# Optimization experiments

Measured on AMD Instinct MI355X. Metric: run time of the kernel, lower is better.

Reference implementation:

```python
import jax, jax.numpy as jnp
import numpy as np

N = 100000
E = 1600000
L = 128   # latent_size
H = 128   # hidden_size
O = 128   # output_size


def setup_inputs() -> dict:
    key = jax.random.key(0)
    ks = jax.random.split(key, 16)
    s = 1.0 / np.sqrt(H)
    inp = {
        "z": jax.random.normal(ks[0], (N, L), dtype=jnp.float32),
        "edge_index": jax.random.randint(ks[1], (2, E), 0, N, dtype=jnp.int64),
        # LSTM params (torch order: i, f, g, o)
        "W_ih": jax.random.uniform(ks[2], (4 * H, L), jnp.float32, -s, s),
        "W_hh": jax.random.uniform(ks[3], (4 * H, H), jnp.float32, -s, s),
        "b_ih": jax.random.uniform(ks[4], (4 * H,), jnp.float32, -s, s),
        "b_hh": jax.random.uniform(ks[5], (4 * H,), jnp.float32, -s, s),
        # GCNConv weights (x @ W + b)
        "W1": jax.random.uniform(ks[6], (H, H), jnp.float32, -s, s),
        "b1": jnp.zeros((H,), jnp.float32),
        "W2": jax.random.uniform(ks[7], (H, H), jnp.float32, -s, s),
        "b2": jnp.zeros((H,), jnp.float32),
        # final Linear
        "W3": jax.random.uniform(ks[8], (O, H), jnp.float32, -s, s),
        "b3": jax.random.uniform(ks[9], (O,), jnp.float32, -s, s),
    }
    return inp


def _gcn_conv(x, W, b, src, dst, norm, n_nodes):
    # x: [N, H]; src/dst/norm: [E+N] (self-loops included)
    h = x @ W                                   # [N, H] transform first (H==H)
    msg = h[src] * norm[:, None]                # gather + edge scale
    out = jax.ops.segment_sum(msg, dst, num_segments=n_nodes)  # scatter-add
    return out + b


def _lstm_step(z, W_ih, W_hh, b_ih, b_hh):
    # single time-step, h0 = c0 = 0
    gates = z @ W_ih.T + (jnp.zeros((1, H), z.dtype) @ W_hh.T) + b_ih + b_hh
    i, f, g, o = jnp.split(gates, 4, axis=-1)
    c = jax.nn.sigmoid(i) * jnp.tanh(g)         # f * c0 == 0
    return jax.nn.sigmoid(o) * jnp.tanh(c)


def reference(z, edge_index, W_ih, W_hh, b_ih, b_hh, W1, b1, W2, b2, W3, b3):
    n = z.shape[0]
    # add self-loops (PyG GCNConv default)
    loop = jnp.arange(n, dtype=edge_index.dtype)
    src = jnp.concatenate([edge_index[0], loop])
    dst = jnp.concatenate([edge_index[1], loop])
    # symmetric normalization: deg from dst (incoming, incl. self-loop)
    deg = jax.ops.segment_sum(jnp.ones_like(dst, dtype=z.dtype), dst, num_segments=n)
    dinv = jnp.where(deg > 0, jax.lax.rsqrt(deg), 0.0)
    norm = dinv[src] * dinv[dst]

    h = _lstm_step(z, W_ih, W_hh, b_ih, b_hh)
    x = jax.nn.relu(_gcn_conv(h, W1, b1, src, dst, norm, n))
    x = _gcn_conv(x, W2, b2, src, dst, norm, n)
    return jax.nn.relu(x @ W3.T + b3)
```

## Files before the change

kernel.cpp:

```cpp
#include <hip/hip_runtime.h>
#include <math.h>

typedef __attribute__((ext_vector_type(8))) short short8;
typedef __attribute__((ext_vector_type(4))) float floatx4;

#define HDIM 128
#define NPB 256
#define BKMAX 1024
#define CHUNK 8192
#define STAGE_CAP 8192

__device__ __forceinline__ float bf2f(unsigned short u) {
    unsigned int x = ((unsigned int)u) << 16;
    float f;
    __builtin_memcpy(&f, &x, 4);
    return f;
}
__device__ __forceinline__ unsigned short f2bf(float f) {
    unsigned int x;
    __builtin_memcpy(&x, &f, 4);
    unsigned int r = (x + 0x7fffu + ((x >> 16) & 1u)) >> 16;
    return (unsigned short)r;
}
__device__ __forceinline__ void split1(float v, unsigned short& hi, unsigned short& lo) {
    unsigned int x;
    __builtin_memcpy(&x, &v, 4);
    hi = (unsigned short)(x >> 16);
    lo = f2bf(v - bf2f(hi));
}
__device__ __forceinline__ float fast_sigmoid(float x) {
    return 1.0f / (1.0f + __expf(-x));
}
__device__ __forceinline__ float fast_tanh(float x) {
    float ax = fabsf(x);
    float e = __expf(2.0f * ax);
    float t = 1.0f - 2.0f / (e + 1.0f);
    return copysignf(t, x);
}

__device__ __forceinline__ void gload_lds16(const void* g, void* lds) {
    __builtin_amdgcn_global_load_lds(
        (const __attribute__((address_space(1))) unsigned int*)g,
        (__attribute__((address_space(3))) unsigned int*)lds, 16, 0, 0);
}

__global__ void prep_weights_kernel(const float* __restrict__ Wih,
                                    const float* __restrict__ W1,
                                    const float* __restrict__ bih,
                                    const float* __restrict__ bhh,
                                    unsigned short* __restrict__ Wihh, unsigned short* __restrict__ Wihl,
                                    unsigned short* __restrict__ W1h,  unsigned short* __restrict__ W1l,
                                    float* __restrict__ bsum) {
    int i = blockIdx.x * 256 + threadIdx.x;
    unsigned short h, l;
    if (i < 65536) {
        split1(Wih[i], h, l);
        Wihh[i] = h; Wihl[i] = l;
    } else if (i < 81920) {
        int t = i - 65536, r = t >> 7, c = t & 127;
        split1(W1[r * HDIM + c], h, l);
        W1h[c * HDIM + r] = h; W1l[c * HDIM + r] = l;
    } else if (i < 82432) {
        int t = i - 81920;
        bsum[t] = bih[t] + bhh[t];
    }
}

__global__ void prep_w23_kernel(const float* __restrict__ W2,
                                const float* __restrict__ W3,
                                const float* __restrict__ b2,
                                const float* __restrict__ b3,
                                unsigned short* __restrict__ W23h,
                                unsigned short* __restrict__ W23l,
                                float* __restrict__ b23) {
    int i = blockIdx.x * 256 + threadIdx.x;
    if (i < 16384) {
        int n = i >> 7, k = i & 127;
        float s = 0.0f;
#pragma unroll 8
        for (int p = 0; p < 128; ++p)
            s += W2[k * HDIM + p] * W3[n * HDIM + p];
        unsigned short h, l;
        split1(s, h, l);
        W23h[n * HDIM + k] = h;
        W23l[n * HDIM + k] = l;
    } else if (i < 16512) {
        int n = i - 16384;
        float s = b3[n];
#pragma unroll 8
        for (int p = 0; p < 128; ++p)
            s += b2[p] * W3[n * HDIM + p];
        b23[n] = s;
    }
}

__global__ __launch_bounds__(256)
void bucket_hist_kernel(const int* __restrict__ ei, int* __restrict__ bcnt,
                        long E, int K) {
    __shared__ int h[BKMAX];
    const int tid = threadIdx.x;
    for (int i = tid; i < K; i += 256) h[i] = 0;
    __syncthreads();
    const long base = (long)blockIdx.x * CHUNK;
#pragma unroll
    for (int j = 0; j < CHUNK / 256; ++j) {
        long e = base + j * 256 + tid;
        if (e < E) atomicAdd(&h[((unsigned)ei[E + e]) >> 8], 1);
    }
    __syncthreads();
    for (int i = tid; i < K; i += 256) {
        int c = h[i];
        if (c) atomicAdd(&bcnt[i], c);
    }
}

__global__ __launch_bounds__(1024)
void scan_buckets_kernel(const int* __restrict__ bcnt, int* __restrict__ gbase,
                         int* __restrict__ gcur, int* __restrict__ offs,
                         int K, int N, int Etot) {
    __shared__ int buf[1024];
    const int t = threadIdx.x;
    const int v = (t < K) ? bcnt[t] : 0;
    buf[t] = v;
    __syncthreads();
    for (int off = 1; off < 1024; off <<= 1) {
        int x = buf[t];
        int y = (t >= off) ? buf[t - off] : 0;
        __syncthreads();
        buf[t] = x + y;
        __syncthreads();
    }
    if (t < K) { gbase[t] = buf[t] - v; gcur[t] = buf[t] - v; }
    if (t == 0) { gbase[K] = Etot; offs[N] = Etot; }
}

__global__ __launch_bounds__(256)
void pair_scatter_kernel(const int* __restrict__ ei, int* __restrict__ gcur,
                         unsigned int* __restrict__ pairs, long E, int K) {
    __shared__ int h[BKMAX];
    __shared__ int cur[BKMAX];
    const int tid = threadIdx.x;
    for (int i = tid; i < K; i += 256) h[i] = 0;
    __syncthreads();
    const long base = (long)blockIdx.x * CHUNK;
#pragma unroll
    for (int j = 0; j < CHUNK / 256; ++j) {
        long e = base + j * 256 + tid;
        if (e < E) atomicAdd(&h[((unsigned)ei[E + e]) >> 8], 1);
    }
    __syncthreads();
    for (int i = tid; i < K; i += 256) {
        int c = h[i];
        cur[i] = c ? atomicAdd(&gcur[i], c) : 0;
    }
    __syncthreads();
#pragma unroll
    for (int j = 0; j < CHUNK / 256; ++j) {
        long e = base + j * 256 + tid;
        if (e < E) {
            unsigned int s = (unsigned int)ei[e];
            unsigned int d = (unsigned int)ei[E + e];
            int b = d >> 8;
            int pos = atomicAdd(&cur[b], 1);
            pairs[pos] = s | ((d & (NPB - 1)) << 24);
        }
    }
}

__global__ __launch_bounds__(256)
void bucket_csr_kernel(const unsigned int* __restrict__ pairs, const int* __restrict__ gbase,
                       int* __restrict__ offs, float* __restrict__ dinv,
                       int* __restrict__ srclist, int N) {
    __shared__ int cnt[NPB];
    __shared__ int red[NPB];
    __shared__ int cur[NPB];
    __shared__ int stage[STAGE_CAP];
    const int tid = threadIdx.x;
    const int b = blockIdx.x;
    const int node0 = b << 8;
    const int nn = min(NPB, N - node0);
    const int ebeg = gbase[b];
    const int eend = gbase[b + 1];
    const int ne = eend - ebeg;

    cnt[tid] = 0;
    __syncthreads();
    for (int i = tid; i < ne; i += 256)
        atomicAdd(&cnt[pairs[ebeg + i] >> 24], 1);
    __syncthreads();
    const int myc = cnt[tid];
    red[tid] = myc;
    __syncthreads();
    for (int off = 1; off < NPB; off <<= 1) {
        int x = red[tid];
        int y = (tid >= off) ? red[tid - off] : 0;
        __syncthreads();
        red[tid] = x + y;
        __syncthreads();
    }
    const int loff = red[tid] - myc;
    if (tid < nn) {
        offs[node0 + tid] = ebeg + loff;
        dinv[node0 + tid] = rsqrtf((float)myc + 1.0f);
    }
    cur[tid] = loff;
    __syncthreads();

    if (ne <= STAGE_CAP) {
        for (int i = tid; i < ne; i += 256) {
            unsigned int p = pairs[ebeg + i];
            int pos = atomicAdd(&cur[p >> 24], 1);
            stage[pos] = (int)(p & 0xFFFFFFu);
        }
        __syncthreads();
        for (int i = tid; i < ne; i += 256)
            srclist[ebeg + i] = stage[i];
    } else {
        for (int i = tid; i < ne; i += 256) {
            unsigned int p = pairs[ebeg + i];
            int pos = atomicAdd(&cur[p >> 24], 1);
            srclist[ebeg + pos] = (int)(p & 0xFFFFFFu);
        }
    }
}

__device__ __forceinline__ void stage_swz(const unsigned short* __restrict__ g,
                                          long rowBase, long maxRow, int kOff,
                                          unsigned short* lds, int nrows, int tid) {
    const int nchunks = nrows << 3;
    for (int L = tid; L < nchunks; L += 256) {
        int r = L >> 3, cS = L & 7;
        int cG = cS ^ (r & 7);
        long gr = rowBase + r;
        if (gr >= maxRow) gr = maxRow - 1;
        gload_lds16(g + gr * HDIM + kOff + cG * 8, lds + (long)L * 8);
    }
}
__device__ __forceinline__ int swz_off(int r, int c0) {
    return (r * 8 + (c0 ^ (r & 7))) * 8;
}

__global__ __launch_bounds__(256, 4)
void gemm_split(const unsigned short* __restrict__ Ah, const unsigned short* __restrict__ Al,
                const unsigned short* __restrict__ Bh, const unsigned short* __restrict__ Bl,
                float* __restrict__ outf, unsigned short* __restrict__ outb, long M,
                const float* __restrict__ rowScale,
                const float* __restrict__ bias, int mode)
{
    __shared__ unsigned short sBh[128 * 64], sBl[128 * 64];
    const int tid = threadIdx.x;
    const long rowBase = (long)blockIdx.x * 64;

    const int wave = tid >> 6;
    const int lane = tid & 63;
    const int quad = lane >> 4;
    const int l16  = lane & 15;
    const int arow = wave * 16 + l16;
    long ag = rowBase + arow;
    if (ag >= M) ag = M - 1;

    short8 rah[2][2], ral[2][2];
#pragma unroll
    for (int h = 0; h < 2; ++h)
#pragma unroll
        for (int kk = 0; kk < 2; ++kk) {
            const long o = ag * HDIM + h * 64 + kk * 32 + quad * 8;
            rah[h][kk] = *(const short8*)(Ah + o);
            ral[h][kk] = *(const short8*)(Al + o);
        }

    floatx4 acc[8];
#pragma unroll
    for (int i = 0; i < 8; ++i) acc[i] = (floatx4)0.0f;

    for (int h = 0; h < 2; ++h) {
        __syncthreads();
        stage_swz(Bh, 0, 128, h * 64, sBh, 128, tid);
        stage_swz(Bl, 0, 128, h * 64, sBl, 128, tid);
        __syncthreads();
#pragma unroll
        for (int kk = 0; kk < 2; ++kk) {
            const int c0 = kk * 4 + quad;
            short8 ah = rah[h][kk];
            short8 al = ral[h][kk];
#pragma unroll
            for (int ct = 0; ct < 8; ++ct) {
                const int bo = swz_off(ct * 16 + l16, c0);
                short8 bh = *(const short8*)(sBh + bo);
                short8 bl = *(const short8*)(sBl + bo);
                acc[ct] = __builtin_amdgcn_mfma_f32_16x16x32_bf16(ah, bh, acc[ct], 0, 0, 0);
                acc[ct] = __builtin_amdgcn_mfma_f32_16x16x32_bf16(ah, bl, acc[ct], 0, 0, 0);
                acc[ct] = __builtin_amdgcn_mfma_f32_16x16x32_bf16(al, bh, acc[ct], 0, 0, 0);
            }
        }
    }

#pragma unroll
    for (int ct = 0; ct < 8; ++ct) {
#pragma unroll
        for (int r = 0; r < 4; ++r) {
            long m = rowBase + wave * 16 + quad * 4 + r;
            if (m < M) {
                int n = ct * 16 + l16;
                float v = acc[ct][r];
                if (mode == 0) {
                    v *= rowScale[m];
                    outb[m * HDIM + n] = f2bf(v);
                } else {
                    v += bias[n];
                    v = fmaxf(v, 0.0f);
                    outf[m * HDIM + n] = v;
                }
            }
        }
    }
}

__global__ __launch_bounds__(256, 2)
void lstm_gemm_split(const float* __restrict__ Z,
                     const unsigned short* __restrict__ Wh, const unsigned short* __restrict__ Wl,
                     const float* __restrict__ bsum,
                     unsigned short* __restrict__ Hh, unsigned short* __restrict__ Hl, long M)
{
    __shared__ unsigned short sBh[2][128 * 64], sBl[2][128 * 64];
    const int tid = threadIdx.x;
    const long rowBase = (long)blockIdx.x * 64;

    const int wave = tid >> 6;
    const int lane = tid & 63;
    const int quad = lane >> 4;
    const int l16  = lane & 15;
    const int arow = wave * 16 + l16;
    long ag = rowBase + arow;
    if (ag >= M) ag = M - 1;

    short8 rah[2][2], ral[2][2];
#pragma unroll
    for (int h = 0; h < 2; ++h)
#pragma unroll
        for (int kk = 0; kk < 2; ++kk) {
            const float* p = Z + ag * HDIM + h * 64 + kk * 32 + quad * 8;
            float4 f0 = *(const float4*)p;
            float4 f1 = *(const float4*)(p + 4);
            float f[8] = {f0.x, f0.y, f0.z, f0.w, f1.x, f1.y, f1.z, f1.w};
#pragma unroll
            for (int e = 0; e < 8; ++e) {
                unsigned short hi, lo;
                split1(f[e], hi, lo);
                rah[h][kk][e] = (short)hi;
                ral[h][kk][e] = (short)lo;
            }
        }

    auto stage_phase = [&](int ph, int b) {
        const int g = ph >> 1, h = ph & 1;
        const int gateRow = (g == 0) ? 0 : ((g == 1) ? 256 : 384);
        const unsigned short* gh = Wh + (long)gateRow * HDIM + h * 64;
        const unsigned short* gl = Wl + (long)gateRow * HDIM + h * 64;
#pragma unroll
        for (int it = 0; it < 4; ++it) {
            int L = it * 256 + tid;
            int r = L >> 3, cS = L & 7, cG = cS ^ (r & 7);
            gload_lds16(gh + (long)r * HDIM + cG * 8, &sBh[b][L * 8]);
        }
#pragma unroll
        for (int it = 0; it < 4; ++it) {
            int L = it * 256 + tid;
            int r = L >> 3, cS = L & 7, cG = cS ^ (r & 7);
            gload_lds16(gl + (long)r * HDIM + cG * 8, &sBl[b][L * 8]);
        }
    };

    floatx4 acc[8];
    floatx4 st[8];
#pragma unroll
    for (int i = 0; i < 8; ++i) acc[i] = (floatx4)0.0f;

    stage_phase(0, 0);

#pragma unroll
    for (int ph = 0; ph < 6; ++ph) {
        const int b = ph & 1;
        if (ph < 5) stage_phase(ph + 1, b ^ 1);
        if (ph == 2) {
#pragma unroll
            for (int ct = 0; ct < 8; ++ct) {
                const float bb = bsum[ct * 16 + l16];
#pragma unroll
                for (int r = 0; r < 4; ++r)
                    st[ct][r] = fast_sigmoid(acc[ct][r] + bb);
                acc[ct] = (floatx4)0.0f;
            }
        } else if (ph == 4) {
#pragma unroll
            for (int ct = 0; ct < 8; ++ct) {
                const float bb = bsum[256 + ct * 16 + l16];
#pragma unroll
                for (int r = 0; r < 4; ++r) {
                    float cv = st[ct][r] * fast_tanh(acc[ct][r] + bb);
                    st[ct][r] = fast_tanh(cv);
                }
                acc[ct] = (floatx4)0.0f;
            }
        }
        if (ph < 5) asm volatile("s_waitcnt vmcnt(8)" ::: "memory");
        else        asm volatile("s_waitcnt vmcnt(0)" ::: "memory");
        __builtin_amdgcn_s_barrier();
        asm volatile("" ::: "memory");
        const int hh_ = ph & 1;
#pragma unroll
        for (int kk = 0; kk < 2; ++kk) {
            const int c0 = kk * 4 + quad;
            short8 a_h = rah[hh_][kk];
            short8 a_l = ral[hh_][kk];
#pragma unroll
            for (int ct = 0; ct < 8; ++ct) {
                const int bo = swz_off(ct * 16 + l16, c0);
                short8 bh = *(const short8*)(&sBh[b][0] + bo);
                short8 bl = *(const short8*)(&sBl[b][0] + bo);
                acc[ct] = __builtin_amdgcn_mfma_f32_16x16x32_bf16(a_h, bh, acc[ct], 0, 0, 0);
                acc[ct] = __builtin_amdgcn_mfma_f32_16x16x32_bf16(a_h, bl, acc[ct], 0, 0, 0);
                acc[ct] = __builtin_amdgcn_mfma_f32_16x16x32_bf16(a_l, bh, acc[ct], 0, 0, 0);
            }
        }
        asm volatile("s_waitcnt lgkmcnt(0)" ::: "memory");
        __builtin_amdgcn_s_barrier();
        asm volatile("" ::: "memory");
    }

#pragma unroll
    for (int ct = 0; ct < 8; ++ct) {
        const float bb = bsum[384 + ct * 16 + l16];
#pragma unroll
        for (int r = 0; r < 4; ++r) {
            long m = rowBase + wave * 16 + quad * 4 + r;
            if (m < M) {
                float hv = fast_sigmoid(acc[ct][r] + bb) * st[ct][r];
                unsigned short hh, hl;
                split1(hv, hh, hl);
                int n = ct * 16 + l16;
                Hh[m * HDIM + n] = hh;
                Hl[m * HDIM + n] = hl;
            }
        }
    }
}

__global__ __launch_bounds__(256, 4)
void aggregate_kernel(const unsigned short* __restrict__ t, const int* __restrict__ srclist,
                      const int* __restrict__ offs, const float* __restrict__ dinv,
                      const float* __restrict__ bias, int doRelu,
                      unsigned short* __restrict__ Xh, unsigned short* __restrict__ Xl,
                      float* __restrict__ outF, long N)
{
    long node = (long)blockIdx.x * 4 + (threadIdx.x >> 6);
    if (node >= N) return;
    const int lane = threadIdx.x & 63;
    const int c = lane * 2;
    const int beg = offs[node];
    const int end = offs[node + 1];
    float s0[8], s1[8];
#pragma unroll
    for (int q = 0; q < 8; ++q) { s0[q] = 0.0f; s1[q] = 0.0f; }
    int j = beg;
    for (; j + 8 <= end; j += 8) {
        int srcs[8];
#pragma unroll
        for (int q = 0; q < 8; ++q) srcs[q] = srclist[j + q];
        unsigned int p[8];
#pragma unroll
        for (int q = 0; q < 8; ++q) p[q] = *(const unsigned int*)(t + (long)srcs[q] * HDIM + c);
#pragma unroll
        for (int q = 0; q < 8; ++q) {
            s0[q] += bf2f((unsigned short)(p[q] & 0xffffu));
            s1[q] += bf2f((unsigned short)(p[q] >> 16));
        }
    }
    for (; j + 4 <= end; j += 4) {
        int srcs[4];
#pragma unroll
        for (int q = 0; q < 4; ++q) srcs[q] = srclist[j + q];
#pragma unroll
        for (int q = 0; q < 4; ++q) {
            unsigned int p = *(const unsigned int*)(t + (long)srcs[q] * HDIM + c);
            s0[q] += bf2f((unsigned short)(p & 0xffffu));
            s1[q] += bf2f((unsigned short)(p >> 16));
        }
    }
    for (; j < end; ++j) {
        unsigned int p = *(const unsigned int*)(t + (long)srclist[j] * HDIM + c);
        s0[0] += bf2f((unsigned short)(p & 0xffffu));
        s1[0] += bf2f((unsigned short)(p >> 16));
    }
    const unsigned int ps = *(const unsigned int*)(t + node * HDIM + c);
    s0[0] += bf2f((unsigned short)(ps & 0xffffu));
    s1[0] += bf2f((unsigned short)(ps >> 16));
    float a0 = ((s0[0] + s0[1]) + (s0[2] + s0[3])) + ((s0[4] + s0[5]) + (s0[6] + s0[7]));
    float a1 = ((s1[0] + s1[1]) + (s1[2] + s1[3])) + ((s1[4] + s1[5]) + (s1[6] + s1[7]));
    const float d = dinv[node];
    float v0 = d * a0 + bias[c];
    float v1 = d * a1 + bias[c + 1];
    if (outF) {
        v0 = fmaxf(v0, 0.0f);
        v1 = fmaxf(v1, 0.0f);
        float2 o2 = {v0, v1};
        *(float2*)(outF + node * HDIM + c) = o2;
        return;
    }
    if (doRelu) { v0 = fmaxf(v0, 0.0f); v1 = fmaxf(v1, 0.0f); }
    unsigned short h0, l0, h1, l1;
    split1(v0, h0, l0);
    split1(v1, h1, l1);
    *(unsigned int*)(Xh + node * HDIM + c) = (unsigned int)h0 | ((unsigned int)h1 << 16);
    *(unsigned int*)(Xl + node * HDIM + c) = (unsigned int)l0 | ((unsigned int)l1 << 16);
}

extern "C" void kernel_launch(void* const* d_in, const int* in_sizes, int n_in,
                              void* d_out, int out_size, void* d_ws, size_t ws_size,
                              hipStream_t stream)
{
    const float* z   = (const float*)d_in[0];
    const int*   ei  = (const int*)d_in[1];
    const float* Wih = (const float*)d_in[2];
    const float* bih = (const float*)d_in[4];
    const float* bhh = (const float*)d_in[5];
    const float* W1  = (const float*)d_in[6];
    const float* b1  = (const float*)d_in[7];
    const float* W2  = (const float*)d_in[8];
    const float* b2  = (const float*)d_in[9];
    const float* W3  = (const float*)d_in[10];
    const float* b3  = (const float*)d_in[11];
    float* out = (float*)d_out;

    const long N = in_sizes[0] / HDIM;
    const long E = in_sizes[1] / 2;
    const int  K = (int)((N + NPB - 1) / NPB);

    char* ws = (char*)d_ws;
    size_t off = 0;
    auto alloc = [&](size_t bytes) {
        char* p = ws + off;
        off += (bytes + 255) & ~(size_t)255;
        return (void*)p;
    };
    int*   bcnt    = (int*)alloc(K * 4);
    int*   gbase   = (int*)alloc((K + 1) * 4);
    int*   gcur    = (int*)alloc(K * 4);
    int*   offs    = (int*)alloc((N + 1) * 4);
    float* dinv    = (float*)alloc(N * 4);
    unsigned int* pairs = (unsigned int*)alloc(E * 4);
    int*   srclist = (int*)alloc(E * 4);
    unsigned short* P1h = (unsigned short*)alloc(N * HDIM * 2);
    unsigned short* P1l = (unsigned short*)alloc(N * HDIM * 2);
    unsigned short* P2h = (unsigned short*)alloc(N * HDIM * 2);
    unsigned short* P2l = (unsigned short*)alloc(N * HDIM * 2);
    unsigned short* Tb  = (unsigned short*)alloc(N * HDIM * 2);
    unsigned short* Wihh = (unsigned short*)alloc(512 * HDIM * 2);
    unsigned short* Wihl = (unsigned short*)alloc(512 * HDIM * 2);
    unsigned short* W1h  = (unsigned short*)alloc(HDIM * HDIM * 2);
    unsigned short* W1l  = (unsigned short*)alloc(HDIM * HDIM * 2);
    unsigned short* W23h = (unsigned short*)alloc(HDIM * HDIM * 2);
    unsigned short* W23l = (unsigned short*)alloc(HDIM * HDIM * 2);
    float* bsum = (float*)alloc(512 * 4);
    float* b23  = (float*)alloc(HDIM * 4);

    const int gblocks  = (int)((N + 63) / 64);
    const int ablocks  = (int)((N + 3) / 4);
    const int cblocks  = (int)((E + CHUNK - 1) / CHUNK);

    hipMemsetAsync(bcnt, 0, K * 4, stream);
    bucket_hist_kernel<<<cblocks, 256, 0, stream>>>(ei, bcnt, E, K);
    scan_buckets_kernel<<<1, 1024, 0, stream>>>(bcnt, gbase, gcur, offs, K, (int)N, (int)E);
    pair_scatter_kernel<<<cblocks, 256, 0, stream>>>(ei, gcur, pairs, E, K);
    bucket_csr_kernel<<<K, 256, 0, stream>>>(pairs, gbase, offs, dinv, srclist, (int)N);

    prep_weights_kernel<<<322, 256, 0, stream>>>(Wih, W1, bih, bhh,
                                                 Wihh, Wihl, W1h, W1l, bsum);
    prep_w23_kernel<<<65, 256, 0, stream>>>(W2, W3, b2, b3, W23h, W23l, b23);

    lstm_gemm_split<<<gblocks, 256, 0, stream>>>(z, Wihh, Wihl, bsum, P2h, P2l, N);

    gemm_split<<<gblocks, 256, 0, stream>>>(P2h, P2l, W1h, W1l, nullptr, Tb, N, dinv, nullptr, 0);
    aggregate_kernel<<<ablocks, 256, 0, stream>>>(Tb, srclist, offs, dinv, b1, 1,
                                                  P1h, P1l, nullptr, N);

    gemm_split<<<gblocks, 256, 0, stream>>>(P1h, P1l, W23h, W23l, nullptr, Tb, N, dinv, nullptr, 0);
    aggregate_kernel<<<ablocks, 256, 0, stream>>>(Tb, srclist, offs, dinv, b23, 1,
                                                  nullptr, nullptr, out, N);
}
```

Baseline: 440.1 us.

## Fuse LSTM GEMM with first GCN weight GEMM via shared-memory staging

The LSTM output tile (hi/lo bf16 split) now stays in shared memory instead of being written to global buffers. The same block then multiplies it by W1 and writes the dinv-scaled bf16 transform directly. This removes the write and re-read of two N×128 bf16 intermediates and one kernel launch. In exchange the fused kernel does more work per block and reuses its shared buffers, which needs correct synchronization.

```diff
diff --git a/kernel.cpp b/kernel.cpp
--- a/kernel.cpp
+++ b/kernel.cpp
@@ -317,10 +317,11 @@
 }
 
 __global__ __launch_bounds__(256, 2)
-void lstm_gemm_split(const float* __restrict__ Z,
-                     const unsigned short* __restrict__ Wh, const unsigned short* __restrict__ Wl,
-                     const float* __restrict__ bsum,
-                     unsigned short* __restrict__ Hh, unsigned short* __restrict__ Hl, long M)
+void lstm_gemm1_fused(const float* __restrict__ Z,
+                      const unsigned short* __restrict__ Wh, const unsigned short* __restrict__ Wl,
+                      const unsigned short* __restrict__ W1h, const unsigned short* __restrict__ W1l,
+                      const float* __restrict__ bsum, const float* __restrict__ dinv,
+                      unsigned short* __restrict__ Tb, long M)
 {
     __shared__ unsigned short sBh[2][128 * 64], sBl[2][128 * 64];
     const int tid = threadIdx.x;
@@ -433,14 +434,57 @@
         const float bb = bsum[384 + ct * 16 + l16];
 #pragma unroll
         for (int r = 0; r < 4; ++r) {
+            float hv = fast_sigmoid(acc[ct][r] + bb) * st[ct][r];
+            unsigned short hh, hl;
+            split1(hv, hh, hl);
+            int row = wave * 16 + quad * 4 + r;
+            int col = ct * 16 + l16;
+            int c = col >> 3;
+            int sc = (c & 8) | ((c ^ row) & 7);
+            int idx = (row * 16 + sc) * 8 + (col & 7);
+            sBh[0][idx] = hh;
+            sBl[0][idx] = hl;
+        }
+    }
+
+    floatx4 acc2[8];
+#pragma unroll
+    for (int i = 0; i < 8; ++i) acc2[i] = (floatx4)0.0f;
+
+#pragma unroll
+    for (int h2 = 0; h2 < 2; ++h2) {
+        __syncthreads();
+        stage_swz(W1h, 0, 128, h2 * 64, &sBh[1][0], 128, tid);
+        stage_swz(W1l, 0, 128, h2 * 64, &sBl[1][0], 128, tid);
+        __syncthreads();
+#pragma unroll
+        for (int kk = 0; kk < 2; ++kk) {
+            const int cA = h2 * 8 + kk * 4 + quad;
+            const int scA = (cA & 8) | ((cA ^ arow) & 7);
+            short8 a_h = *(const short8*)(&sBh[0][(arow * 16 + scA) * 8]);
+            short8 a_l = *(const short8*)(&sBl[0][(arow * 16 + scA) * 8]);
+            const int c0 = kk * 4 + quad;
+#pragma unroll
+            for (int ct = 0; ct < 8; ++ct) {
+                const int bo = swz_off(ct * 16 + l16, c0);
+                short8 bh = *(const short8*)(&sBh[1][0] + bo);
+                short8 bl = *(const short8*)(&sBl[1][0] + bo);
+                acc2[ct] = __builtin_amdgcn_mfma_f32_16x16x32_bf16(a_h, bh, acc2[ct], 0, 0, 0);
+                acc2[ct] = __builtin_amdgcn_mfma_f32_16x16x32_bf16(a_h, bl, acc2[ct], 0, 0, 0);
+                acc2[ct] = __builtin_amdgcn_mfma_f32_16x16x32_bf16(a_l, bh, acc2[ct], 0, 0, 0);
+            }
+        }
+    }
+
+#pragma unroll
+    for (int ct = 0; ct < 8; ++ct) {
+#pragma unroll
+        for (int r = 0; r < 4; ++r) {
             long m = rowBase + wave * 16 + quad * 4 + r;
             if (m < M) {
-                float hv = fast_sigmoid(acc[ct][r] + bb) * st[ct][r];
-                unsigned short hh, hl;
-                split1(hv, hh, hl);
                 int n = ct * 16 + l16;
-                Hh[m * HDIM + n] = hh;
-                Hl[m * HDIM + n] = hl;
+                float v = acc2[ct][r] * dinv[m];
+                Tb[m * HDIM + n] = f2bf(v);
             }
         }
     }
@@ -552,8 +596,6 @@
     int*   srclist = (int*)alloc(E * 4);
     unsigned short* P1h = (unsigned short*)alloc(N * HDIM * 2);
     unsigned short* P1l = (unsigned short*)alloc(N * HDIM * 2);
-    unsigned short* P2h = (unsigned short*)alloc(N * HDIM * 2);
-    unsigned short* P2l = (unsigned short*)alloc(N * HDIM * 2);
     unsigned short* Tb  = (unsigned short*)alloc(N * HDIM * 2);
     unsigned short* Wihh = (unsigned short*)alloc(512 * HDIM * 2);
     unsigned short* Wihl = (unsigned short*)alloc(512 * HDIM * 2);
@@ -578,9 +620,9 @@
                                                  Wihh, Wihl, W1h, W1l, bsum);
     prep_w23_kernel<<<65, 256, 0, stream>>>(W2, W3, b2, b3, W23h, W23l, b23);
 
-    lstm_gemm_split<<<gblocks, 256, 0, stream>>>(z, Wihh, Wihl, bsum, P2h, P2l, N);
-
-    gemm_split<<<gblocks, 256, 0, stream>>>(P2h, P2l, W1h, W1l, nullptr, Tb, N, dinv, nullptr, 0);
+    lstm_gemm1_fused<<<gblocks, 256, 0, stream>>>(z, Wihh, Wihl, W1h, W1l,
+                                                  bsum, dinv, Tb, N);
+
     aggregate_kernel<<<ablocks, 256, 0, stream>>>(Tb, srclist, offs, dinv, b1, 1,
                                                   P1h, P1l, nullptr, N);
 
```

Measured after the change: 420.4 us. 1.05x faster.
